# Optimization experiments

Hardware: AMD Instinct MI355X
Metric: run time of the kernel (lower is better)

Reference implementation:

```python
import jax, jax.numpy as jnp
import numpy as np

B, CIN, H, W = 32, 16, 32, 128
COUT = 128


def _run_direction(x_hwbc, p):
    # x_hwbc: (H, W, B, CIN); scan order is raster (top-to-bottom, left-to-right).
    # Predecessors: dim0 = cell above (previous row), dim1 = cell to the left.
    xi = jnp.einsum('hwbc,oc->hwbo', x_hwbc, p['w_ii'])
    xf = jnp.einsum('hwbc,oc->hwbo', x_hwbc, p['w_if'])
    xg = jnp.einsum('hwbc,oc->hwbo', x_hwbc, p['w_ig'])
    xo = jnp.einsum('hwbc,oc->hwbo', x_hwbc, p['w_io'])
    Wdim, Bdim = x_hwbc.shape[1], x_hwbc.shape[2]
    O = p['w_hi'].shape[0]
    ws0, ws1 = p['ws'][0], p['ws'][1]

    def branch(xi_, xf_, xg_, xo_, c, h):
        i = jax.nn.sigmoid(xi_ + h @ p['w_hi'].T + p['b_i'])
        f = jax.nn.sigmoid(xf_ + h @ p['w_hf'].T + p['b_f'])
        g = jnp.tanh(xg_ + h @ p['w_hg'].T + p['b_g'])
        o = jax.nn.sigmoid(xo_ + h @ p['w_ho'].T + p['b_o'])
        cn = f * c + i * g
        return cn, o * jnp.tanh(cn)

    def col_step(carry, inp):
        c_left, h_left = carry                      # (B, O)
        xi_, xf_, xg_, xo_, c_top, h_top = inp      # each (B, O)
        c0, h0 = branch(xi_, xf_, xg_, xo_, c_top, h_top)   # vertical predecessor
        c1, h1 = branch(xi_, xf_, xg_, xo_, c_left, h_left) # horizontal predecessor
        ct = ws0 * c0 + ws1 * c1 + p['bias']
        ht = ws0 * h0 + ws1 * h1 + p['bias']
        return (ct, ht), (ct, ht)

    def row_step(carry, row):
        c_top, h_top = carry                        # (W, B, O)
        xi_r, xf_r, xg_r, xo_r = row
        z = jnp.zeros((Bdim, O), xi_r.dtype)
        _, (c_row, h_row) = jax.lax.scan(col_step, (z, z), (xi_r, xf_r, xg_r, xo_r, c_top, h_top))
        return (c_row, h_row), h_row

    z_row = jnp.zeros((Wdim, Bdim, O), x_hwbc.dtype)
    _, h_all = jax.lax.scan(row_step, (z_row, z_row), (xi, xf, xg, xo))
    return h_all  # (H, W, B, O)


def _forward(x, w_ii, w_hi, b_i, w_if, w_hf, b_f, w_ig, w_hg, b_g,
             w_io, w_ho, b_o, weighted_sum, bias):
    # Four scan directions realized by flipping the grid (lr_tb, rl_tb, lr_bt, rl_bt).
    x_hwbc = jnp.transpose(x, (2, 3, 0, 1))  # (H, W, B, CIN)
    flips = [(False, False), (False, True), (True, False), (True, True)]
    outs = []
    for d, (fy, fx) in enumerate(flips):
        xd = x_hwbc
        if fy:
            xd = xd[::-1]
        if fx:
            xd = xd[:, ::-1]
        p = {'w_ii': w_ii[d], 'w_hi': w_hi[d], 'b_i': b_i[d],
             'w_if': w_if[d], 'w_hf': w_hf[d], 'b_f': b_f[d],
             'w_ig': w_ig[d], 'w_hg': w_hg[d], 'b_g': b_g[d],
             'w_io': w_io[d], 'w_ho': w_ho[d], 'b_o': b_o[d],
             'ws': weighted_sum[d], 'bias': bias[d]}
        h = _run_direction(xd, p)
        if fy:
            h = h[::-1]
        if fx:
            h = h[:, ::-1]
        outs.append(h)
    h4 = jnp.stack(outs)                      # (4, H, W, B, O)
    return jnp.transpose(h4, (0, 4, 3, 1, 2)) # (4, O, B, H, W)


def setup_inputs() -> dict:
    key = jax.random.key(0)
    ks = jax.random.split(key, 16)
    xw = lambda k: jax.random.normal(k, (4, COUT, CIN), jnp.float32) * 0.05
    hw = lambda k: jax.random.normal(k, (4, COUT, COUT), jnp.float32) * 0.05
    bb = lambda k: jax.random.normal(k, (4, COUT), jnp.float32) * 0.05
    return {
        'x': jax.random.normal(ks[0], (B, CIN, H, W), jnp.float32),
        'w_ii': xw(ks[1]), 'w_hi': hw(ks[2]), 'b_i': bb(ks[3]),
        'w_if': xw(ks[4]), 'w_hf': hw(ks[5]), 'b_f': bb(ks[6]),
        'w_ig': xw(ks[7]), 'w_hg': hw(ks[8]), 'b_g': bb(ks[9]),
        'w_io': xw(ks[10]), 'w_ho': hw(ks[11]), 'b_o': bb(ks[12]),
        'weighted_sum': jax.random.uniform(ks[13], (4, 2), jnp.float32),
        'bias': bb(ks[14]),
    }


def reference(x, w_ii, w_hi, b_i, w_if, w_hf, b_f, w_ig, w_hg, b_g,
              w_io, w_ho, b_o, weighted_sum, bias):
    return _forward(x, w_ii, w_hi, b_i, w_if, w_hf, b_f, w_ig, w_hg, b_g,
                    w_io, w_ho, b_o, weighted_sum, bias)
```

## Files before the change

### kernel.cpp

```cpp
#include <hip/hip_runtime.h>

#define Hh 32
#define Ww 128
#define BB 32
#define CC 16
#define OO 128
#define DEPTH 4
#define SPIN_CAP (1 << 23)
#define FSTRIDE 32

typedef __attribute__((ext_vector_type(8))) short short8;
typedef __attribute__((ext_vector_type(4))) float f32x4;

__device__ inline short f2bf(float f) {
    unsigned u = __builtin_bit_cast(unsigned, f);
    unsigned r = (u + 0x7FFFu + ((u >> 16) & 1u)) >> 16;
    return (short)r;
}
__device__ inline float bf2f(short s) {
    unsigned u = ((unsigned)(unsigned short)s) << 16;
    return __builtin_bit_cast(float, u);
}
__device__ inline float rcp_(float x) { return __builtin_amdgcn_rcpf(x); }
__device__ inline float sigm(float x) {
    return rcp_(1.f + __builtin_amdgcn_exp2f(-1.442695041f * x));
}
__device__ inline float tanh_(float x) {
    return 1.f - 2.f * rcp_(__builtin_amdgcn_exp2f(2.885390082f * x) + 1.f);
}

__device__ inline unsigned long long aload64(const unsigned long long* p) {
    return __hip_atomic_load(p, __ATOMIC_RELAXED, __HIP_MEMORY_SCOPE_AGENT);
}
__device__ inline void astore64(unsigned long long* p, unsigned long long v) {
    __hip_atomic_store(p, v, __ATOMIC_RELAXED, __HIP_MEMORY_SCOPE_AGENT);
}
__device__ inline short aloadS(const short* p) {
    return __hip_atomic_load(p, __ATOMIC_RELAXED, __HIP_MEMORY_SCOPE_AGENT);
}
__device__ inline int aloadI(const int* p) {
    return __hip_atomic_load(p, __ATOMIC_RELAXED, __HIP_MEMORY_SCOPE_AGENT);
}
__device__ inline void astoreI(int* p, int v) {
    __hip_atomic_store(p, v, __ATOMIC_RELAXED, __HIP_MEMORY_SCOPE_AGENT);
}

__global__ void mdlstm_init(const float* __restrict__ x, short* __restrict__ xT,
                            int* __restrict__ flags) {
    int idx = blockIdx.x * 256 + threadIdx.x;
    if (blockIdx.x < 64) flags[idx] = 0;
    int w = idx & 127;
    int h = (idx >> 7) & 31;
    int c = (idx >> 12) & 15;
    int b = idx >> 16;
    float v = x[idx];
    xT[((h * Ww + w) * BB + b) * CC + c] = f2bf(v);
}

__global__ void __launch_bounds__(512, 1) mdlstm_main(
    const short* __restrict__ xT,
    const float* __restrict__ w_ii, const float* __restrict__ w_hi, const float* __restrict__ b_i,
    const float* __restrict__ w_if, const float* __restrict__ w_hf, const float* __restrict__ b_f,
    const float* __restrict__ w_ig, const float* __restrict__ w_hg, const float* __restrict__ b_g,
    const float* __restrict__ w_io, const float* __restrict__ w_ho, const float* __restrict__ b_o,
    const float* __restrict__ wsum, const float* __restrict__ bias,
    short* __restrict__ hring, float* __restrict__ cring,
    int* __restrict__ prog, int* __restrict__ cons,
    float* __restrict__ out)
{
    const int chain = blockIdx.x & 7;
    const int r     = blockIdx.x >> 3;
    const int d     = chain >> 1;
    const int s     = chain & 1;
    const int b0    = s * 16;
    const bool fy   = (d >= 2);
    const bool fx   = (d & 1);
    const int hh    = fy ? (Hh - 1 - r) : r;

    const int tid  = threadIdx.x;
    const int wv   = tid >> 6;
    const int lane = tid & 63;
    const int lr   = lane & 15;
    const int lh   = lane >> 4;
    const int on   = wv * 16 + lr;

    __shared__ short stage[OO * 256];

    const float* whp[4] = {w_hi, w_hf, w_hg, w_ho};
    const float* wip[4] = {w_ii, w_if, w_ig, w_io};
    short8 whf[4][4];
    short8 wif_[4];
#pragma unroll
    for (int g = 0; g < 4; ++g) {
#pragma unroll
        for (int kt = 0; kt < 4; ++kt) {
            const float* p = whp[g] + ((d * OO + on) * OO + kt * 32 + lh * 8);
            short8 f;
#pragma unroll
            for (int j = 0; j < 8; ++j) f[j] = f2bf(p[j]);
            whf[g][kt] = f;
        }
        short8 fi = (short8)(short)0;
        if (lh < 2) {
            const float* p = wip[g] + ((d * OO + on) * CC + lh * 8);
#pragma unroll
            for (int j = 0; j < 8; ++j) fi[j] = f2bf(p[j]);
        }
        wif_[g] = fi;
    }

    const float bi  = b_i[d * OO + on];
    const float bf_ = b_f[d * OO + on];
    const float bg_ = b_g[d * OO + on];
    const float bo_ = b_o[d * OO + on];
    const float bb_ = bias[d * OO + on];
    const float ws0 = wsum[d * 2 + 0];
    const float ws1 = wsum[d * 2 + 1];

    int* topf      = prog + ((d * 32 + (r - 1)) * 2 + s) * FSTRIDE;
    int* myprog    = prog + ((d * 32 + r) * 2 + s) * FSTRIDE;
    int* mycons    = cons + ((d * 32 + r) * 2 + s) * FSTRIDE;
    int* consnext  = cons + ((d * 32 + (r + 1)) * 2 + s) * FSTRIDE;

    const int rb_me  = (d * 32 + r) * DEPTH * BB * OO;
    const int rb_top = (d * 32 + (r - 1)) * DEPTH * BB * OO;

    short8 hLf[4];
#pragma unroll
    for (int kt = 0; kt < 4; ++kt) hLf[kt] = (short8)(short)0;
    float cL[4] = {0.f, 0.f, 0.f, 0.f};

    int top_seen = 0, cons_seen = 0;
    const f32x4 zacc = {0.f, 0.f, 0.f, 0.f};

    for (int wsc = 0; wsc < Ww; ++wsc) {
        const int ww    = fx ? (Ww - 1 - wsc) : wsc;
        const int slot  = wsc & (DEPTH - 1);
        const int wslot = ww & 15;

        short8 xf = (short8)(short)0;
        if (lh < 2) {
            const short* p = xT + ((hh * Ww + ww) * BB + b0 + lr) * CC + lh * 8;
            xf = *(const short8*)p;
        }

        short8 hTf[4];
        float cT[4];
        if (r > 0) {
            const int need = wsc + 1;
            if (top_seen < need) {
                int spin = 0;
                while (top_seen < need && spin < SPIN_CAP) {
                    int v = 0;
                    if (lane == 0) v = aloadI(topf);
                    v = __shfl(v, 0, 64);
                    if (v < need) { __builtin_amdgcn_s_sleep(1); ++spin; } else top_seen = v;
                }
            }
            const short* hb = hring + rb_top + slot * OO * BB + b0 + lr;
#pragma unroll
            for (int kt = 0; kt < 4; ++kt) {
                short8 f;
#pragma unroll
                for (int jj = 0; jj < 8; ++jj)
                    f[jj] = aloadS(hb + (kt * 32 + lh * 8 + jj) * BB);
                hTf[kt] = f;
            }
            const unsigned long long* cp =
                (const unsigned long long*)(cring + rb_top + slot * OO * BB + on * BB + b0 + lh * 4);
            union { unsigned long long q; float f[2]; } c01, c23;
            c01.q = aload64(cp);
            c23.q = aload64(cp + 1);
            cT[0] = c01.f[0]; cT[1] = c01.f[1]; cT[2] = c23.f[0]; cT[3] = c23.f[1];
        } else {
#pragma unroll
            for (int kt = 0; kt < 4; ++kt) hTf[kt] = (short8)(short)0;
#pragma unroll
            for (int j = 0; j < 4; ++j) cT[j] = 0.f;
        }

        f32x4 ax[4], accL[4], accT[4];
#pragma unroll
        for (int g = 0; g < 4; ++g)
            ax[g] = __builtin_amdgcn_mfma_f32_16x16x32_bf16(xf, wif_[g], zacc, 0, 0, 0);
#pragma unroll
        for (int g = 0; g < 4; ++g) {
            f32x4 a = ax[g];
#pragma unroll
            for (int kt = 0; kt < 4; ++kt)
                a = __builtin_amdgcn_mfma_f32_16x16x32_bf16(hLf[kt], whf[g][kt], a, 0, 0, 0);
            accL[g] = a;
        }
#pragma unroll
        for (int g = 0; g < 4; ++g) {
            f32x4 a = ax[g];
#pragma unroll
            for (int kt = 0; kt < 4; ++kt)
                a = __builtin_amdgcn_mfma_f32_16x16x32_bf16(hTf[kt], whf[g][kt], a, 0, 0, 0);
            accT[g] = a;
        }

        float ctv[4];
        union { short sh[4]; unsigned long long q; } hpack;
#pragma unroll
        for (int j = 0; j < 4; ++j) {
            float iT = sigm(accT[0][j] + bi);
            float fT = sigm(accT[1][j] + bf_);
            float gT = tanh_(accT[2][j] + bg_);
            float oT = sigm(accT[3][j] + bo_);
            float c0 = fT * cT[j] + iT * gT;
            float h0 = oT * tanh_(c0);

            float iL = sigm(accL[0][j] + bi);
            float fL = sigm(accL[1][j] + bf_);
            float gL = tanh_(accL[2][j] + bg_);
            float oL = sigm(accL[3][j] + bo_);
            float c1 = fL * cL[j] + iL * gL;
            float h1 = oL * tanh_(c1);

            float ct = ws0 * c0 + ws1 * c1 + bb_;
            float ht = ws0 * h0 + ws1 * h1 + bb_;
            cL[j] = ct;
            ctv[j] = ct;
            hpack.sh[j] = f2bf(ht);
        }

        {
            const int g_on = (on >> 3) & 15;
            *(unsigned long long*)&stage[on * 256 + ((wslot ^ g_on) << 4) + lh * 4] = hpack.q;
        }

        if (r < 31 && wsc >= DEPTH) {
            const int need = wsc - DEPTH + 1;
            if (cons_seen < need) {
                int spin = 0;
                while (cons_seen < need && spin < SPIN_CAP) {
                    int v = 0;
                    if (lane == 0) v = aloadI(consnext);
                    v = __shfl(v, 0, 64);
                    if (v < need) { __builtin_amdgcn_s_sleep(1); ++spin; } else cons_seen = v;
                }
            }
        }

        if (r < 31) {
            astore64((unsigned long long*)(hring + rb_me + slot * OO * BB + on * BB + b0 + lh * 4),
                     hpack.q);
            union { float f[2]; unsigned long long q; } p01, p23;
            p01.f[0] = ctv[0]; p01.f[1] = ctv[1];
            p23.f[0] = ctv[2]; p23.f[1] = ctv[3];
            unsigned long long* cp =
                (unsigned long long*)(cring + rb_me + slot * OO * BB + on * BB + b0 + lh * 4);
            astore64(cp, p01.q);
            astore64(cp + 1, p23.q);
        }

        __syncthreads();

        if (tid == 0) {
            if (r < 31) astoreI(myprog, wsc + 1);
            if (r > 0)  astoreI(mycons, wsc + 1);
        }

        if (r > 0 && wsc < Ww - 1) {
            int v = 0;
            if (lane == 0) v = aloadI(topf);
            v = __shfl(v, 0, 64);
            if (v > top_seen) top_seen = v;
        }

#pragma unroll
        for (int kt = 0; kt < 4; ++kt) {
            const int col = ((wslot ^ (kt * 4 + lh)) << 4) + lr;
            short8 f;
#pragma unroll
            for (int jj = 0; jj < 8; ++jj)
                f[jj] = stage[(kt * 32 + lh * 8 + jj) * 256 + col];
            hLf[kt] = f;
        }

        if ((wsc & 15) == 15) {
            const int wbase = ww & ~15;
            const int q  = tid & 3;
            const int r0 = tid >> 2;
#pragma unroll
            for (int i = 0; i < 16; ++i) {
                const int row = r0 + (i << 7);
                const int o = row >> 4;
                const int b = row & 15;
                const int go = (o >> 3) & 15;
                f32x4 v;
#pragma unroll
                for (int k = 0; k < 4; ++k)
                    v[k] = bf2f(stage[o * 256 + (((q * 4 + k) ^ go) << 4) + b]);
                float* op = out + ((size_t)((d * OO + o) * BB + b0 + b)) * (Hh * Ww)
                                + hh * Ww + wbase + q * 4;
                *(f32x4*)op = v;
            }
            __syncthreads();
        }
    }
}

extern "C" void kernel_launch(void* const* d_in, const int* in_sizes, int n_in,
                              void* d_out, int out_size, void* d_ws, size_t ws_size,
                              hipStream_t stream) {
    (void)in_sizes; (void)n_in; (void)out_size; (void)ws_size;

    const float* x     = (const float*)d_in[0];
    const float* w_ii  = (const float*)d_in[1];
    const float* w_hi  = (const float*)d_in[2];
    const float* b_i   = (const float*)d_in[3];
    const float* w_if  = (const float*)d_in[4];
    const float* w_hf  = (const float*)d_in[5];
    const float* b_f   = (const float*)d_in[6];
    const float* w_ig  = (const float*)d_in[7];
    const float* w_hg  = (const float*)d_in[8];
    const float* b_g   = (const float*)d_in[9];
    const float* w_io  = (const float*)d_in[10];
    const float* w_ho  = (const float*)d_in[11];
    const float* b_o   = (const float*)d_in[12];
    const float* wsum  = (const float*)d_in[13];
    const float* bias  = (const float*)d_in[14];
    float* outp        = (float*)d_out;

    char* ws = (char*)d_ws;
    int*   flags  = (int*)ws;
    short* xTp    = (short*)(ws + (64u << 10));
    short* hringp = (short*)(ws + (64u << 10) + (4u << 20));
    float* cringp = (float*)(ws + (64u << 10) + (8u << 20));
    int*   progp  = flags;
    int*   consp  = flags + 256 * FSTRIDE;

    hipLaunchKernelGGL(mdlstm_init, dim3(8192), dim3(256), 0, stream, x, xTp, flags);

    mdlstm_main<<<dim3(256), dim3(512), 0, stream>>>(
        xTp,
        w_ii, w_hi, b_i,
        w_if, w_hf, b_f,
        w_ig, w_hg, b_g,
        w_io, w_ho, b_o,
        wsum, bias,
        hringp, cringp, progp, consp,
        outp);
}
```

Before: 1.164 ms.

## Batch inter-row handoff into column pairs with per-wave atomic progress counters

Cross-row producer/consumer synchronisation now runs once per pair of columns. On even columns the consumer waits on a counter and prefetches the top row's h/c for two columns at once; on odd columns it reuses the buffered values. The single tid-0 flag store after the block barrier is replaced by per-wave atomic fetch-add counters (release for progress, relaxed for consumption), so each wave publishes independently. The h ring layout is transposed to batch-major so the consumer reads 64-bit vectors instead of scalar 16-bit atomics, but the producer now issues four 16-bit atomic stores. This adds register pressure and coarser pipelining between rows, which could delay downstream rows.

```diff
diff --git a/kernel.cpp b/kernel.cpp
--- a/kernel.cpp
+++ b/kernel.cpp
@@ -35,14 +35,17 @@
 __device__ inline void astore64(unsigned long long* p, unsigned long long v) {
     __hip_atomic_store(p, v, __ATOMIC_RELAXED, __HIP_MEMORY_SCOPE_AGENT);
 }
-__device__ inline short aloadS(const short* p) {
-    return __hip_atomic_load(p, __ATOMIC_RELAXED, __HIP_MEMORY_SCOPE_AGENT);
+__device__ inline void astore16(short* p, short v) {
+    __hip_atomic_store(p, v, __ATOMIC_RELAXED, __HIP_MEMORY_SCOPE_AGENT);
 }
 __device__ inline int aloadI(const int* p) {
     return __hip_atomic_load(p, __ATOMIC_RELAXED, __HIP_MEMORY_SCOPE_AGENT);
 }
-__device__ inline void astoreI(int* p, int v) {
-    __hip_atomic_store(p, v, __ATOMIC_RELAXED, __HIP_MEMORY_SCOPE_AGENT);
+__device__ inline void afadd_rel(int* p) {
+    (void)__hip_atomic_fetch_add(p, 1, __ATOMIC_RELEASE, __HIP_MEMORY_SCOPE_AGENT);
+}
+__device__ inline void afadd_rlx(int* p) {
+    (void)__hip_atomic_fetch_add(p, 1, __ATOMIC_RELAXED, __HIP_MEMORY_SCOPE_AGENT);
 }
 
 __global__ void mdlstm_init(const float* __restrict__ x, short* __restrict__ xT,
@@ -130,13 +133,20 @@
     for (int kt = 0; kt < 4; ++kt) hLf[kt] = (short8)(short)0;
     float cL[4] = {0.f, 0.f, 0.f, 0.f};
 
+    short8 hTfB[4];
+#pragma unroll
+    for (int kt = 0; kt < 4; ++kt) hTfB[kt] = (short8)(short)0;
+    float cTB[4] = {0.f, 0.f, 0.f, 0.f};
+
     int top_seen = 0, cons_seen = 0;
     const f32x4 zacc = {0.f, 0.f, 0.f, 0.f};
 
+#pragma unroll 2
     for (int wsc = 0; wsc < Ww; ++wsc) {
         const int ww    = fx ? (Ww - 1 - wsc) : wsc;
         const int slot  = wsc & (DEPTH - 1);
         const int wslot = ww & 15;
+        const bool evenc = ((wsc & 1) == 0);
 
         short8 xf = (short8)(short)0;
         if (lh < 2) {
@@ -147,31 +157,51 @@
         short8 hTf[4];
         float cT[4];
         if (r > 0) {
-            const int need = wsc + 1;
-            if (top_seen < need) {
-                int spin = 0;
-                while (top_seen < need && spin < SPIN_CAP) {
-                    int v = 0;
-                    if (lane == 0) v = aloadI(topf);
-                    v = __shfl(v, 0, 64);
-                    if (v < need) { __builtin_amdgcn_s_sleep(1); ++spin; } else top_seen = v;
+            if (evenc) {
+                const int need = 4 * wsc + 8;
+                if (top_seen < need) {
+                    int spin = 0;
+                    while (top_seen < need && spin < SPIN_CAP) {
+                        int v = 0;
+                        if (lane == 0) v = aloadI(topf);
+                        v = __shfl(v, 0, 64);
+                        if (v < need) { __builtin_amdgcn_s_sleep(1); ++spin; } else top_seen = v;
+                    }
                 }
+                const short* hb = hring + rb_top + slot * BB * OO + (b0 + lr) * OO;
+#pragma unroll
+                for (int kt = 0; kt < 4; ++kt) {
+                    const unsigned long long* p = (const unsigned long long*)(hb + kt * 32 + lh * 8);
+                    union { unsigned long long q[2]; short8 v; } u;
+                    u.q[0] = aload64(p);
+                    u.q[1] = aload64(p + 1);
+                    hTf[kt] = u.v;
+                }
+                const short* hb2 = hb + BB * OO;
+#pragma unroll
+                for (int kt = 0; kt < 4; ++kt) {
+                    const unsigned long long* p = (const unsigned long long*)(hb2 + kt * 32 + lh * 8);
+                    union { unsigned long long q[2]; short8 v; } u;
+                    u.q[0] = aload64(p);
+                    u.q[1] = aload64(p + 1);
+                    hTfB[kt] = u.v;
+                }
+                const unsigned long long* cp =
+                    (const unsigned long long*)(cring + rb_top + slot * OO * BB + on * BB + b0 + lh * 4);
+                union { unsigned long long q; float f[2]; } c01, c23;
+                c01.q = aload64(cp);
+                c23.q = aload64(cp + 1);
+                cT[0] = c01.f[0]; cT[1] = c01.f[1]; cT[2] = c23.f[0]; cT[3] = c23.f[1];
+                const unsigned long long* cp2 = cp + (OO * BB / 2);
+                c01.q = aload64(cp2);
+                c23.q = aload64(cp2 + 1);
+                cTB[0] = c01.f[0]; cTB[1] = c01.f[1]; cTB[2] = c23.f[0]; cTB[3] = c23.f[1];
+            } else {
+#pragma unroll
+                for (int kt = 0; kt < 4; ++kt) hTf[kt] = hTfB[kt];
+#pragma unroll
+                for (int j = 0; j < 4; ++j) cT[j] = cTB[j];
             }
-            const short* hb = hring + rb_top + slot * OO * BB + b0 + lr;
-#pragma unroll
-            for (int kt = 0; kt < 4; ++kt) {
-                short8 f;
-#pragma unroll
-                for (int jj = 0; jj < 8; ++jj)
-                    f[jj] = aloadS(hb + (kt * 32 + lh * 8 + jj) * BB);
-                hTf[kt] = f;
-            }
-            const unsigned long long* cp =
-                (const unsigned long long*)(cring + rb_top + slot * OO * BB + on * BB + b0 + lh * 4);
-            union { unsigned long long q; float f[2]; } c01, c23;
-            c01.q = aload64(cp);
-            c23.q = aload64(cp + 1);
-            cT[0] = c01.f[0]; cT[1] = c01.f[1]; cT[2] = c23.f[0]; cT[3] = c23.f[1];
         } else {
 #pragma unroll
             for (int kt = 0; kt < 4; ++kt) hTf[kt] = (short8)(short)0;
@@ -230,8 +260,10 @@
             *(unsigned long long*)&stage[on * 256 + ((wslot ^ g_on) << 4) + lh * 4] = hpack.q;
         }
 
-        if (r < 31 && wsc >= DEPTH) {
-            const int need = wsc - DEPTH + 1;
+        if (r > 0 && !evenc && lane == 0) afadd_rlx(mycons);
+
+        if (r < 31 && evenc && wsc >= DEPTH) {
+            const int need = 4 * wsc - 8;
             if (cons_seen < need) {
                 int spin = 0;
                 while (cons_seen < need && spin < SPIN_CAP) {
@@ -244,8 +276,10 @@
         }
 
         if (r < 31) {
-            astore64((unsigned long long*)(hring + rb_me + slot * OO * BB + on * BB + b0 + lh * 4),
-                     hpack.q);
+#pragma unroll
+            for (int j = 0; j < 4; ++j)
+                astore16(hring + rb_me + slot * BB * OO + (b0 + lh * 4 + j) * OO + on,
+                         hpack.sh[j]);
             union { float f[2]; unsigned long long q; } p01, p23;
             p01.f[0] = ctv[0]; p01.f[1] = ctv[1];
             p23.f[0] = ctv[2]; p23.f[1] = ctv[3];
@@ -255,14 +289,11 @@
             astore64(cp + 1, p23.q);
         }
 
+        if (r < 31 && !evenc && lane == 0) afadd_rel(myprog);
+
         __syncthreads();
 
-        if (tid == 0) {
-            if (r < 31) astoreI(myprog, wsc + 1);
-            if (r > 0)  astoreI(mycons, wsc + 1);
-        }
-
-        if (r > 0 && wsc < Ww - 1) {
+        if (r > 0 && !evenc && wsc < Ww - 1) {
             int v = 0;
             if (lane == 0) v = aloadI(topf);
             v = __shfl(v, 0, 64);
```

Measured after the change: 2.990 ms. 2.57x slower.

## Batch row-to-row handshakes to every two columns with paired top-state prefetch

Applied to the files above, without the earlier changes.

Each row block now waits for and publishes progress flags only on every second column. On even columns it loads the top neighbor's h and c for two consecutive columns and reuses the second set on the odd column. This halves the global-memory flag polling and flag stores, and the cross-row latency exposure that goes with them. In exchange it adds a one-column coarser wavefront lag between rows, higher register pressure from the extra buffered fragments, and ring-slot reuse constraints that depend on DEPTH.

```diff
diff --git a/kernel.cpp b/kernel.cpp
--- a/kernel.cpp
+++ b/kernel.cpp
@@ -130,13 +130,20 @@
     for (int kt = 0; kt < 4; ++kt) hLf[kt] = (short8)(short)0;
     float cL[4] = {0.f, 0.f, 0.f, 0.f};
 
+    short8 hTfB[4];
+#pragma unroll
+    for (int kt = 0; kt < 4; ++kt) hTfB[kt] = (short8)(short)0;
+    float cTB[4] = {0.f, 0.f, 0.f, 0.f};
+
     int top_seen = 0, cons_seen = 0;
     const f32x4 zacc = {0.f, 0.f, 0.f, 0.f};
 
+#pragma unroll 2
     for (int wsc = 0; wsc < Ww; ++wsc) {
         const int ww    = fx ? (Ww - 1 - wsc) : wsc;
         const int slot  = wsc & (DEPTH - 1);
         const int wslot = ww & 15;
+        const bool evenc = ((wsc & 1) == 0);
 
         short8 xf = (short8)(short)0;
         if (lh < 2) {
@@ -147,31 +154,51 @@
         short8 hTf[4];
         float cT[4];
         if (r > 0) {
-            const int need = wsc + 1;
-            if (top_seen < need) {
-                int spin = 0;
-                while (top_seen < need && spin < SPIN_CAP) {
-                    int v = 0;
-                    if (lane == 0) v = aloadI(topf);
-                    v = __shfl(v, 0, 64);
-                    if (v < need) { __builtin_amdgcn_s_sleep(1); ++spin; } else top_seen = v;
+            if (evenc) {
+                const int need = wsc + 2;
+                if (top_seen < need) {
+                    int spin = 0;
+                    while (top_seen < need && spin < SPIN_CAP) {
+                        int v = 0;
+                        if (lane == 0) v = aloadI(topf);
+                        v = __shfl(v, 0, 64);
+                        if (v < need) { __builtin_amdgcn_s_sleep(1); ++spin; } else top_seen = v;
+                    }
                 }
+                const short* hb = hring + rb_top + slot * OO * BB + b0 + lr;
+#pragma unroll
+                for (int kt = 0; kt < 4; ++kt) {
+                    short8 f;
+#pragma unroll
+                    for (int jj = 0; jj < 8; ++jj)
+                        f[jj] = aloadS(hb + (kt * 32 + lh * 8 + jj) * BB);
+                    hTf[kt] = f;
+                }
+                const short* hb2 = hb + OO * BB;
+#pragma unroll
+                for (int kt = 0; kt < 4; ++kt) {
+                    short8 f;
+#pragma unroll
+                    for (int jj = 0; jj < 8; ++jj)
+                        f[jj] = aloadS(hb2 + (kt * 32 + lh * 8 + jj) * BB);
+                    hTfB[kt] = f;
+                }
+                const unsigned long long* cp =
+                    (const unsigned long long*)(cring + rb_top + slot * OO * BB + on * BB + b0 + lh * 4);
+                union { unsigned long long q; float f[2]; } c01, c23;
+                c01.q = aload64(cp);
+                c23.q = aload64(cp + 1);
+                cT[0] = c01.f[0]; cT[1] = c01.f[1]; cT[2] = c23.f[0]; cT[3] = c23.f[1];
+                const unsigned long long* cp2 = cp + (OO * BB / 2);
+                c01.q = aload64(cp2);
+                c23.q = aload64(cp2 + 1);
+                cTB[0] = c01.f[0]; cTB[1] = c01.f[1]; cTB[2] = c23.f[0]; cTB[3] = c23.f[1];
+            } else {
+#pragma unroll
+                for (int kt = 0; kt < 4; ++kt) hTf[kt] = hTfB[kt];
+#pragma unroll
+                for (int j = 0; j < 4; ++j) cT[j] = cTB[j];
             }
-            const short* hb = hring + rb_top + slot * OO * BB + b0 + lr;
-#pragma unroll
-            for (int kt = 0; kt < 4; ++kt) {
-                short8 f;
-#pragma unroll
-                for (int jj = 0; jj < 8; ++jj)
-                    f[jj] = aloadS(hb + (kt * 32 + lh * 8 + jj) * BB);
-                hTf[kt] = f;
-            }
-            const unsigned long long* cp =
-                (const unsigned long long*)(cring + rb_top + slot * OO * BB + on * BB + b0 + lh * 4);
-            union { unsigned long long q; float f[2]; } c01, c23;
-            c01.q = aload64(cp);
-            c23.q = aload64(cp + 1);
-            cT[0] = c01.f[0]; cT[1] = c01.f[1]; cT[2] = c23.f[0]; cT[3] = c23.f[1];
         } else {
 #pragma unroll
             for (int kt = 0; kt < 4; ++kt) hTf[kt] = (short8)(short)0;
@@ -230,8 +257,8 @@
             *(unsigned long long*)&stage[on * 256 + ((wslot ^ g_on) << 4) + lh * 4] = hpack.q;
         }
 
-        if (r < 31 && wsc >= DEPTH) {
-            const int need = wsc - DEPTH + 1;
+        if (r < 31 && evenc && wsc >= DEPTH) {
+            const int need = wsc - 2;
             if (cons_seen < need) {
                 int spin = 0;
                 while (cons_seen < need && spin < SPIN_CAP) {
@@ -257,12 +284,12 @@
 
         __syncthreads();
 
-        if (tid == 0) {
+        if (!evenc && tid == 0) {
             if (r < 31) astoreI(myprog, wsc + 1);
             if (r > 0)  astoreI(mycons, wsc + 1);
         }
 
-        if (r > 0 && wsc < Ww - 1) {
+        if (r > 0 && !evenc && wsc < Ww - 1) {
             int v = 0;
             if (lane == 0) v = aloadI(topf);
             v = __shfl(v, 0, 64);
```

New measurement: 1.107 ms. 4.9% less time.
